# Performance work log

Measured on AMD Instinct MI355X. Metric: run time of the kernel, lower is better.

The kernel has to match this reference:

```python
import jax, jax.numpy as jnp
import numpy as np

B, CIN, COUT, H, W = 16, 128, 128, 64, 64
K1, K2, DIL = 3, 3, 1
PAD0 = DIL * (K1 - 1) // 2
PAD1 = DIL * (K2 - 1) // 2
L = H * W


def setup_inputs() -> dict:
    key = jax.random.key(0)
    k1, k2, k3, k4, k5 = jax.random.split(key, 5)
    x = jax.random.normal(k1, (B, CIN, H, W), dtype=jnp.float32)
    # binary per-pixel mask over kernel taps, broadcast over batch*channels
    mask = (jax.random.uniform(k2, (1, K1 * K2, L)) < 0.5).astype(jnp.float32)
    fan_in = CIN * K1 * K2
    bound = 1.0 / np.sqrt(fan_in)
    weight = jax.random.uniform(k3, (COUT, CIN, K1, K2), jnp.float32, -bound, bound)
    mask_weight = jax.random.uniform(k4, (COUT, K1, K2), jnp.float32, -bound, bound)
    bias = jax.random.uniform(k5, (COUT,), jnp.float32, -bound, bound)
    return {"x": x, "mask": mask, "weight": weight, "mask_weight": mask_weight, "bias": bias}


def reference(x, mask, weight, mask_weight, bias):
    # im2col: [B, CIN*K1*K2, H, W]; channel ordering (cin, k1, k2) matches torch unfold
    patches = jax.lax.conv_general_dilated_patches(
        x, (K1, K2), (1, 1), [(PAD0, PAD0), (PAD1, PAD1)], rhs_dilation=(DIL, DIL))
    p = patches.reshape(B, CIN, K1 * K2, L)
    p = p * mask[:, None, :, :]          # mask [1, K, L] broadcasts over B and CIN
    p = p.reshape(B, CIN * K1 * K2, L)
    out = jnp.einsum('ok,bkl->bol', weight.reshape(COUT, -1), p)
    out = out + bias[None, :, None]
    out = out + jnp.einsum('ok,mkl->mol', mask_weight.reshape(COUT, -1), mask)
    return out.reshape(B, COUT, H, W)
```

## Files before the change

kernel.cpp:

```cpp
#include <hip/hip_runtime.h>
#include <stdint.h>

#define B_    16
#define CIN_  128
#define COUT_ 128
#define H_    64
#define W_    64
#define L_    4096
#define KK_   1152
#define PW_   66
#define PPIX_ (PW_ * PW_)

typedef unsigned short u16;
typedef __bf16 bf16x8 __attribute__((ext_vector_type(8)));
typedef float  floatx4 __attribute__((ext_vector_type(4)));
typedef uint32_t u32x4 __attribute__((ext_vector_type(4)));

typedef const __attribute__((address_space(1))) uint32_t* gptr_t;
typedef __attribute__((address_space(3))) uint32_t*       lptr_t;

__device__ __forceinline__ void async_copy16(const void* g, void* l) {
    __builtin_amdgcn_global_load_lds((gptr_t)g, (lptr_t)l, 16, 0, 0);
}

__device__ __forceinline__ u16 f2bf(float f) {
    uint32_t u = __builtin_bit_cast(uint32_t, f);
    uint32_t r = u + 0x7FFFu + ((u >> 16) & 1u);
    return (u16)(r >> 16);
}

__global__ void lmc_prep_kernel(const float* __restrict__ x,
                                const float* __restrict__ mask, const float* __restrict__ mw,
                                const float* __restrict__ bias, const float* __restrict__ w,
                                u16* __restrict__ xTp, float* __restrict__ mb,
                                u16* __restrict__ wb2) {
    const int bid = blockIdx.x, tid = threadIdx.x;
    if (bid < 1024) {
        __shared__ u16 tile[64][CIN_ + 8];
        const int b = bid >> 6;
        const int y = bid & 63;

        {
            const int c  = tid >> 1;
            const int x0 = (tid & 1) * 32;
            const float* src = x + ((size_t)b * CIN_ + c) * L_ + y * 64 + x0;
            #pragma unroll
            for (int j = 0; j < 32; j += 4) {
                float4 v = *reinterpret_cast<const float4*>(src + j);
                tile[x0 + j + 0][c] = f2bf(v.x);
                tile[x0 + j + 1][c] = f2bf(v.y);
                tile[x0 + j + 2][c] = f2bf(v.z);
                tile[x0 + j + 3][c] = f2bf(v.w);
            }
        }
        __syncthreads();

        u16* dstrow = xTp + ((size_t)(b * PW_ + (y + 1)) * PW_) * CIN_;
        {
            const int xx   = tid >> 2;
            const int cseg = (tid & 3) * 32;
            u16* dst = dstrow + (size_t)(xx + 1) * CIN_ + cseg;
            #pragma unroll
            for (int i = 0; i < 32; i += 8) {
                *reinterpret_cast<uint4*>(dst + i) =
                    *reinterpret_cast<const uint4*>(&tile[xx][cseg + i]);
            }
        }
        const uint4 z = {0u, 0u, 0u, 0u};
        if (tid < 32) {
            const int pix = (tid >> 4) ? 65 : 0;
            *reinterpret_cast<uint4*>(dstrow + (size_t)pix * CIN_ + (tid & 15) * 8) = z;
        }
        if (y == 0 || y == 63) {
            u16* brow = xTp + ((size_t)(b * PW_ + (y == 0 ? 0 : 65)) * PW_) * CIN_;
            for (int i = tid; i < (PW_ * CIN_) / 8; i += 256)
                reinterpret_cast<uint4*>(brow)[i] = z;
        }
    } else if (bid < 1152) {
        const int o = bid - 1024;
        float m[9];
        #pragma unroll
        for (int k = 0; k < 9; ++k) m[k] = mw[o * 9 + k];
        const float bs = bias[o];
        for (int l = tid; l < L_; l += 256) {
            float s = bs;
            #pragma unroll
            for (int k = 0; k < 9; ++k) s += m[k] * mask[k * L_ + l];
            mb[o * L_ + l] = s;
        }
    } else {
        const int base = (bid - 1152) * 2304;
        #pragma unroll
        for (int i = 0; i < 9; ++i) {
            const int e = base + i * 256 + tid;
            const int k = e >> 14;
            const int rem = e & 16383;
            const int o = rem >> 7, c = rem & 127;
            wb2[e] = f2bf(w[(size_t)o * KK_ + c * 9 + k]);
        }
    }
}

#define SH_(k) (((k) / 3 - 1) * 66 + ((k) % 3 - 1))

#define GSTEP(cur, nxt, k, ks, DO_LOAD, kn, ksn)                              \
    do {                                                                      \
        if (DO_LOAD) {                                                        \
            const int shn = SH_(kn);                                          \
            _Pragma("unroll")                                                 \
            for (int j = 0; j < 4; ++j) {                                     \
                const int pixn  = pix0[j] + shn;                              \
                const int slotn = ((ksn) * 4 + quad) ^ (pixn & 7);            \
                nxt[j] = *reinterpret_cast<const bf16x8*>(                    \
                            &W_lds[pixn * 128 + slotn * 8]);                  \
            }                                                                 \
        }                                                                     \
        bf16x8 bm[4];                                                         \
        _Pragma("unroll")                                                     \
        for (int j = 0; j < 4; ++j) {                                         \
            u32x4 t = __builtin_bit_cast(u32x4, cur[j]);                      \
            t &= kp[j];                                                       \
            bm[j] = __builtin_bit_cast(bf16x8, t);                            \
        }                                                                     \
        _Pragma("unroll")                                                     \
        for (int i = 0; i < 4; ++i)                                           \
            _Pragma("unroll")                                                 \
            for (int j = 0; j < 4; ++j)                                       \
                acc[i][j] = __builtin_amdgcn_mfma_f32_16x16x32_bf16(          \
                    af[i][ks], bm[j], acc[i][j], 0, 0, 0);                    \
        _Pragma("unroll")                                                     \
        for (int i = 0; i < 4; ++i)                                           \
            af[i][ks] = *reinterpret_cast<const bf16x8*>(                     \
                wkn + arow[i] + (ks) * 32);                                   \
    } while (0)

__global__ __launch_bounds__(256, 2)
void lmc_gemm_kernel(const u16* __restrict__ xTp, const u16* __restrict__ wb2,
                     const float* __restrict__ mask, const float* __restrict__ mb,
                     float* __restrict__ out) {
    __shared__ u16 W_lds[264 * 128];

    const int flat    = blockIdx.x;
    const int logical = (flat & 7) * 64 + (flat >> 3);
    const int b       = logical >> 5;
    const int lt      = logical & 31;
    const int Y       = lt * 2;
    const int l0      = lt * 128;

    const int tid  = threadIdx.x;
    const int lane = tid & 63;
    const int wv   = tid >> 6;
    const int wm   = (wv >> 1) * 64;
    const int wn   = (wv & 1) * 64;
    const int lrow = lane & 15;
    const int quad = lane >> 4;

    {
        const char* xw = (const char*)xTp + ((size_t)(b * PW_ + Y) * PW_) * 256;
        for (int t = wv; t < 66; t += 4) {
            const int p    = t * 4 + quad;
            const int srcc = lrow ^ (p & 7);
            async_copy16(xw + (size_t)p * 256 + srcc * 16,
                         (char*)W_lds + t * 1024);
        }
    }

    int arow[4];
    #pragma unroll
    for (int i = 0; i < 4; ++i)
        arow[i] = (wm + i * 16 + lrow) * 128 + quad * 8;

    bf16x8 af[4][4];
    #pragma unroll
    for (int i = 0; i < 4; ++i)
        #pragma unroll
        for (int ks = 0; ks < 4; ++ks)
            af[i][ks] = *reinterpret_cast<const bf16x8*>(wb2 + arow[i] + ks * 32);

    int pix0[4];
    uint64_t bits = 0;
    #pragma unroll
    for (int j = 0; j < 4; ++j) {
        const int ll = wn + j * 16 + lrow;
        pix0[j] = ((ll >> 6) + 1) * 66 + (ll & 63) + 1;
        const int lg = l0 + ll;
        #pragma unroll
        for (int k = 0; k < 9; ++k)
            if (mask[k * L_ + lg] != 0.0f) bits |= (1ull << (k * 4 + j));
    }

    floatx4 acc[4][4];
    #pragma unroll
    for (int i = 0; i < 4; ++i)
        #pragma unroll
        for (int j = 0; j < 4; ++j)
            acc[i][j] = (floatx4){0.f, 0.f, 0.f, 0.f};

    __syncthreads();

    bf16x8 bA[4], bB[4];
    {
        const int sh0 = SH_(0);
        #pragma unroll
        for (int j = 0; j < 4; ++j) {
            const int pix  = pix0[j] + sh0;
            const int slot = quad ^ (pix & 7);
            bA[j] = *reinterpret_cast<const bf16x8*>(&W_lds[pix * 128 + slot * 8]);
        }
    }

    #pragma unroll
    for (int k = 0; k < 9; ++k) {
        const u16* wkn = wb2 + ((k < 8) ? (k + 1) : 8) * 16384;
        uint32_t kp[4];
        #pragma unroll
        for (int j = 0; j < 4; ++j)
            kp[j] = 0u - (uint32_t)((bits >> (k * 4 + j)) & 1ull);

        GSTEP(bA, bB, k, 0, true,      k,     1);
        GSTEP(bB, bA, k, 1, true,      k,     2);
        GSTEP(bA, bB, k, 2, true,      k,     3);
        GSTEP(bB, bA, k, 3, (k < 8),   k + 1, 0);
    }

    #pragma unroll
    for (int i = 0; i < 4; ++i) {
        #pragma unroll
        for (int j = 0; j < 4; ++j) {
            const int l = l0 + wn + j * 16 + lrow;
            #pragma unroll
            for (int r = 0; r < 4; ++r) {
                const int o = wm + i * 16 + quad * 4 + r;
                out[((size_t)b * COUT_ + o) * L_ + l] = acc[i][j][r] + mb[o * L_ + l];
            }
        }
    }
}

extern "C" void kernel_launch(void* const* d_in, const int* in_sizes, int n_in,
                              void* d_out, int out_size, void* d_ws, size_t ws_size,
                              hipStream_t stream) {
    const float* x      = (const float*)d_in[0];
    const float* mask   = (const float*)d_in[1];
    const float* weight = (const float*)d_in[2];
    const float* mw     = (const float*)d_in[3];
    const float* bias   = (const float*)d_in[4];
    float* out = (float*)d_out;

    char* ws = (char*)d_ws;
    u16*   xTp = (u16*)ws;
    u16*   wb2 = (u16*)(ws + 17842176);
    float* mb  = (float*)(ws + 17842176 + 294912);

    lmc_prep_kernel<<<1216, 256, 0, stream>>>(x, mask, mw, bias, weight, xTp, mb, wb2);
    lmc_gemm_kernel<<<512, 256, 0, stream>>>(xTp, wb2, mask, mb, out);
}
```

Before: 142.0 us.

## Split GEMM tile across eight waves with smaller per-wave N and A prefetch

Doubles the GEMM block to 512 threads so each wave computes a 64x32 tile instead of 64x64. The A-fragment register buffer shrinks from four k-slices to a two-deep rolling prefetch from global memory, which cuts register pressure so more waves can be resident to hide latency. In exchange, each A fragment is loaded by twice as many waves and the ratio of MFMA work to loads per wave drops.

```diff
diff --git a/kernel.cpp b/kernel.cpp
--- a/kernel.cpp
+++ b/kernel.cpp
@@ -103,38 +103,44 @@
 
 #define SH_(k) (((k) / 3 - 1) * 66 + ((k) % 3 - 1))
 
-#define GSTEP(cur, nxt, k, ks, DO_LOAD, kn, ksn)                              \
+#define GSTEP(k, ks, cur, nxt)                                                \
     do {                                                                      \
-        if (DO_LOAD) {                                                        \
-            const int shn = SH_(kn);                                          \
+        const int g_ = (k) * 4 + (ks);                                        \
+        if (g_ < 35) {                                                        \
+            const int gn_  = g_ + 1;                                          \
+            const int shn_ = SH_(gn_ >> 2);                                   \
             _Pragma("unroll")                                                 \
-            for (int j = 0; j < 4; ++j) {                                     \
-                const int pixn  = pix0[j] + shn;                              \
-                const int slotn = ((ksn) * 4 + quad) ^ (pixn & 7);            \
+            for (int j = 0; j < 2; ++j) {                                     \
+                const int pixn  = pix0[j] + shn_;                             \
+                const int slotn = ((gn_ & 3) * 4 + quad) ^ (pixn & 7);        \
                 nxt[j] = *reinterpret_cast<const bf16x8*>(                    \
                             &W_lds[pixn * 128 + slotn * 8]);                  \
             }                                                                 \
         }                                                                     \
-        bf16x8 bm[4];                                                         \
+        bf16x8 bm[2];                                                         \
         _Pragma("unroll")                                                     \
-        for (int j = 0; j < 4; ++j) {                                         \
+        for (int j = 0; j < 2; ++j) {                                         \
             u32x4 t = __builtin_bit_cast(u32x4, cur[j]);                      \
-            t &= kp[j];                                                       \
+            t &= (0u - (uint32_t)((bits >> ((k) * 2 + j)) & 1u));             \
             bm[j] = __builtin_bit_cast(bf16x8, t);                            \
         }                                                                     \
         _Pragma("unroll")                                                     \
         for (int i = 0; i < 4; ++i)                                           \
             _Pragma("unroll")                                                 \
-            for (int j = 0; j < 4; ++j)                                       \
+            for (int j = 0; j < 2; ++j)                                       \
                 acc[i][j] = __builtin_amdgcn_mfma_f32_16x16x32_bf16(          \
-                    af[i][ks], bm[j], acc[i][j], 0, 0, 0);                    \
-        _Pragma("unroll")                                                     \
-        for (int i = 0; i < 4; ++i)                                           \
-            af[i][ks] = *reinterpret_cast<const bf16x8*>(                     \
-                wkn + arow[i] + (ks) * 32);                                   \
+                    af2[i][(ks) & 1], bm[j], acc[i][j], 0, 0, 0);             \
+        {                                                                     \
+            const int gr_ = (g_ + 2 > 35) ? 35 : g_ + 2;                      \
+            const int ro_ = (gr_ >> 2) * 16384 + (gr_ & 3) * 32;              \
+            _Pragma("unroll")                                                 \
+            for (int i = 0; i < 4; ++i)                                       \
+                af2[i][(ks) & 1] = *reinterpret_cast<const bf16x8*>(          \
+                    wb2 + ro_ + arow[i]);                                     \
+        }                                                                     \
     } while (0)
 
-__global__ __launch_bounds__(256, 2)
+__global__ __launch_bounds__(512, 4)
 void lmc_gemm_kernel(const u16* __restrict__ xTp, const u16* __restrict__ wb2,
                      const float* __restrict__ mask, const float* __restrict__ mb,
                      float* __restrict__ out) {
@@ -150,14 +156,14 @@
     const int tid  = threadIdx.x;
     const int lane = tid & 63;
     const int wv   = tid >> 6;
-    const int wm   = (wv >> 1) * 64;
-    const int wn   = (wv & 1) * 64;
+    const int wm   = (wv >> 2) * 64;
+    const int wn   = (wv & 3) * 32;
     const int lrow = lane & 15;
     const int quad = lane >> 4;
 
     {
         const char* xw = (const char*)xTp + ((size_t)(b * PW_ + Y) * PW_) * 256;
-        for (int t = wv; t < 66; t += 4) {
+        for (int t = wv; t < 66; t += 8) {
             const int p    = t * 4 + quad;
             const int srcc = lrow ^ (p & 7);
             async_copy16(xw + (size_t)p * 256 + srcc * 16,
@@ -170,39 +176,39 @@
     for (int i = 0; i < 4; ++i)
         arow[i] = (wm + i * 16 + lrow) * 128 + quad * 8;
 
-    bf16x8 af[4][4];
-    #pragma unroll
-    for (int i = 0; i < 4; ++i)
-        #pragma unroll
-        for (int ks = 0; ks < 4; ++ks)
-            af[i][ks] = *reinterpret_cast<const bf16x8*>(wb2 + arow[i] + ks * 32);
-
-    int pix0[4];
-    uint64_t bits = 0;
-    #pragma unroll
-    for (int j = 0; j < 4; ++j) {
+    bf16x8 af2[4][2];
+    #pragma unroll
+    for (int i = 0; i < 4; ++i) {
+        af2[i][0] = *reinterpret_cast<const bf16x8*>(wb2 + arow[i]);
+        af2[i][1] = *reinterpret_cast<const bf16x8*>(wb2 + arow[i] + 32);
+    }
+
+    int pix0[2];
+    uint32_t bits = 0;
+    #pragma unroll
+    for (int j = 0; j < 2; ++j) {
         const int ll = wn + j * 16 + lrow;
         pix0[j] = ((ll >> 6) + 1) * 66 + (ll & 63) + 1;
         const int lg = l0 + ll;
         #pragma unroll
         for (int k = 0; k < 9; ++k)
-            if (mask[k * L_ + lg] != 0.0f) bits |= (1ull << (k * 4 + j));
-    }
-
-    floatx4 acc[4][4];
+            if (mask[k * L_ + lg] != 0.0f) bits |= (1u << (k * 2 + j));
+    }
+
+    floatx4 acc[4][2];
     #pragma unroll
     for (int i = 0; i < 4; ++i)
         #pragma unroll
-        for (int j = 0; j < 4; ++j)
+        for (int j = 0; j < 2; ++j)
             acc[i][j] = (floatx4){0.f, 0.f, 0.f, 0.f};
 
     __syncthreads();
 
-    bf16x8 bA[4], bB[4];
+    bf16x8 bA[2], bB[2];
     {
         const int sh0 = SH_(0);
         #pragma unroll
-        for (int j = 0; j < 4; ++j) {
+        for (int j = 0; j < 2; ++j) {
             const int pix  = pix0[j] + sh0;
             const int slot = quad ^ (pix & 7);
             bA[j] = *reinterpret_cast<const bf16x8*>(&W_lds[pix * 128 + slot * 8]);
@@ -211,22 +217,16 @@
 
     #pragma unroll
     for (int k = 0; k < 9; ++k) {
-        const u16* wkn = wb2 + ((k < 8) ? (k + 1) : 8) * 16384;
-        uint32_t kp[4];
-        #pragma unroll
-        for (int j = 0; j < 4; ++j)
-            kp[j] = 0u - (uint32_t)((bits >> (k * 4 + j)) & 1ull);
-
-        GSTEP(bA, bB, k, 0, true,      k,     1);
-        GSTEP(bB, bA, k, 1, true,      k,     2);
-        GSTEP(bA, bB, k, 2, true,      k,     3);
-        GSTEP(bB, bA, k, 3, (k < 8),   k + 1, 0);
+        GSTEP(k, 0, bA, bB);
+        GSTEP(k, 1, bB, bA);
+        GSTEP(k, 2, bA, bB);
+        GSTEP(k, 3, bB, bA);
     }
 
     #pragma unroll
     for (int i = 0; i < 4; ++i) {
         #pragma unroll
-        for (int j = 0; j < 4; ++j) {
+        for (int j = 0; j < 2; ++j) {
             const int l = l0 + wn + j * 16 + lrow;
             #pragma unroll
             for (int r = 0; r < 4; ++r) {
@@ -253,5 +253,5 @@
     float* mb  = (float*)(ws + 17842176 + 294912);
 
     lmc_prep_kernel<<<1216, 256, 0, stream>>>(x, mask, mw, bias, weight, xTp, mb, wb2);
-    lmc_gemm_kernel<<<512, 256, 0, stream>>>(xTp, wb2, mask, mb, out);
-}
+    lmc_gemm_kernel<<<512, 512, 0, stream>>>(xTp, wb2, mask, mb, out);
+}
```

New measurement: 167.3 us. +17.8%, slower.
